# Optimization experiments

Measured on AMD Instinct MI355X. Metric: run time of the kernel, lower is better.

## Reference

```python
import jax, jax.numpy as jnp
import numpy as np

H = 8          # num_heads
NUM_SEEDS = 4  # num_seeds (T = T0 + NUM_SEEDS in training/non_trivial)
NEG_INF = float('-inf')


def setup_inputs() -> dict:
    key = jax.random.key(0)
    ks = jax.random.split(key, 9)
    B, T, L, C = 4, 16, 64, 512
    T0 = T - NUM_SEEDS
    x = jax.random.normal(ks[0], (B, T0 * L, C), dtype=jnp.float32)
    x_ctx = jax.random.normal(ks[1], (B, T, L, C), dtype=jnp.float32)
    dx_ctx = jax.random.normal(ks[2], (B, T, L, C), dtype=jnp.float32)
    ctx_mask = jax.random.randint(ks[3], (B, T), 0, 2).astype(jnp.bool_)
    s = 1.0 / np.sqrt(C)
    qkv_w = jax.random.normal(ks[4], (3 * C, C), dtype=jnp.float32) * s
    k_w = jax.random.normal(ks[5], (C, C), dtype=jnp.float32) * s
    v_w = jax.random.normal(ks[6], (C, C), dtype=jnp.float32) * s
    proj_w = jax.random.normal(ks[7], (C, C), dtype=jnp.float32) * s
    proj_b = jax.random.normal(ks[8], (C,), dtype=jnp.float32) * 0.01
    return {"x": x, "x_ctx": x_ctx, "dx_ctx": dx_ctx, "ctx_mask": ctx_mask,
            "qkv_w": qkv_w, "k_w": k_w, "v_w": v_w, "proj_w": proj_w,
            "proj_b": proj_b}


def reference(x, x_ctx, dx_ctx, ctx_mask, qkv_w, k_w, v_w, proj_w, proj_b):
    B, T, L, C = x_ctx.shape
    T0 = x.shape[1] // L
    hd = C // H
    scale = hd ** (-0.5)

    # qkv for the current (self) tokens: [3, B, H, T0*L, hd]
    qkv = (x @ qkv_w.T).reshape(B, T0 * L, 3, H, hd).transpose(2, 0, 3, 1, 4)
    q, k, v = qkv[0], qkv[1], qkv[2]

    # context keys/values: [B, H, T*L, hd]
    k_ctx = (dx_ctx.reshape(B, T * L, C) @ k_w.T).reshape(B, T * L, H, hd).transpose(0, 2, 1, 3)
    v_ctx = (x_ctx.reshape(B, T * L, C) @ v_w.T).reshape(B, T * L, H, hd).transpose(0, 2, 1, 3)

    # cross-context scores: [B, H, T0*L, T, L]
    attn = (jnp.einsum('bhqd,bhkd->bhqk', q, k_ctx) * scale).reshape(B, H, T0 * L, T, L)

    # context mask: drop whole context frames where ctx_mask is False
    attn = jnp.where(ctx_mask[:, None, None, :, None], attn, NEG_INF)

    # non-trivial temporal mask (training): query frame i can't attend to
    # context frame i + num_seeds
    nt = (jnp.arange(T0)[:, None] + NUM_SEEDS) == jnp.arange(T)[None, :]  # [T0, T]
    attn6 = attn.reshape(B, H, T0, L, T, L)
    attn6 = jnp.where(nt[None, None, :, None, :, None], NEG_INF, attn6)
    attn = attn6.reshape(B, H, T0 * L, T, L)

    # per-frame self attention scores: [B, H, T0, L, L] -> [B, H, T0*L, 1, L]
    q6 = q.reshape(B, H, T0, L, hd)
    k6 = k.reshape(B, H, T0, L, hd)
    self_attn = (jnp.einsum('bhtqd,bhtkd->bhtqk', q6, k6) * scale).reshape(B, H, T0 * L, 1, L)

    # joint softmax over (T+1)*L keys
    attn = jnp.concatenate([attn, self_attn], axis=-2).reshape(B, H, T0 * L, (T + 1) * L)
    attn = jax.nn.softmax(attn, axis=-1)

    # split back: cross part @ v_ctx, self part @ v (per frame)
    out = jnp.einsum('bhqk,bhkd->bhqd', attn[:, :, :, :-L], v_ctx)
    a_self = attn[:, :, :, -L:].reshape(B, H, T0, L, L)
    v6 = v.reshape(B, H, T0, L, hd)
    out = out + jnp.einsum('bhtqk,bhtkd->bhtqd', a_self, v6).reshape(B, H, T0 * L, hd)

    out = out.transpose(0, 2, 1, 3).reshape(B, T0 * L, C)
    return out @ proj_w.T + proj_b
```

## Files before the change

kernel.cpp:

```cpp
#include <hip/hip_runtime.h>
#include <hip/hip_bf16.h>

typedef __attribute__((ext_vector_type(8))) short bf16x8;
typedef __attribute__((ext_vector_type(4))) float f32x4;

#define BB 4
#define TT 16
#define NT0 12
#define LL 64
#define CC 512
#define HH 8
#define HD 64
#define NQ (NT0*LL)
#define NCTX (TT*LL)

#define GPTR(x) ((__attribute__((address_space(1))) void*)(x))
#define SPTR(x) ((__attribute__((address_space(3))) void*)(x))

__device__ __forceinline__ float bf2f(ushort u) {
  union { unsigned int i; float f; } x; x.i = ((unsigned int)u) << 16; return x.f;
}
__device__ __forceinline__ ushort f2bf(float f) {
  union { float f; unsigned int i; } x; x.f = f;
  unsigned int r = x.i + 0x7fffu + ((x.i >> 16) & 1u);
  return (ushort)(r >> 16);
}

__global__ __launch_bounds__(256) void cvt_all(const float* __restrict__ w0,
                                               const float* __restrict__ w1,
                                               const float* __restrict__ w2,
                                               const float* __restrict__ w3,
                                               const float* __restrict__ x,
                                               const float* __restrict__ xc,
                                               const float* __restrict__ dxc,
                                               ushort* __restrict__ dst) {
  long i = (long)blockIdx.x * 256 + threadIdx.x;
  const float* src; long off;
  if (i < 196608)       { src = w0;  off = 0; }
  else if (i < 262144)  { src = w1;  off = 196608; }
  else if (i < 327680)  { src = w2;  off = 262144; }
  else if (i < 393216)  { src = w3;  off = 327680; }
  else if (i < 786432)  { src = x;   off = 393216; }
  else if (i < 1310720) { src = xc;  off = 786432; }
  else                  { src = dxc; off = 1310720; }
  f32x4 v = *(const f32x4*)(src + (i - off) * 4);
  ushort4 o = { f2bf(v[0]), f2bf(v[1]), f2bf(v[2]), f2bf(v[3]) };
  *(ushort4*)(dst + i * 4) = o;
}

__device__ __forceinline__ void gemm128_mac(const ushort* __restrict__ A,
                                            const ushort* __restrict__ W,
                                            int mt, int nt, ushort* lds,
                                            f32x4* acc) {
  int t = threadIdx.x;
  ushort* ldsA = lds;
  ushort* ldsW = lds + 4096;

  int p0 = t, p1 = t + 256;
  int r0 = p0 >> 2, r1 = p1 >> 2;
  int c0 = (p0 & 3) ^ ((r0 >> 1) & 3);
  int c1 = (p1 & 3) ^ ((r1 >> 1) & 3);
  const ushort* ga0 = A + (size_t)(mt * 128 + r0) * 512 + c0 * 8;
  const ushort* ga1 = A + (size_t)(mt * 128 + r1) * 512 + c1 * 8;
  const ushort* gw0 = W + (size_t)(nt * 128 + r0) * 512 + c0 * 8;
  const ushort* gw1 = W + (size_t)(nt * 128 + r1) * 512 + c1 * 8;
  ushort* la0 = ldsA + p0 * 8;
  ushort* la1 = ldsA + p1 * 8;
  ushort* lw0 = ldsW + p0 * 8;
  ushort* lw1 = ldsW + p1 * 8;

  int lane = t & 63, l15 = lane & 15, kg = lane >> 4;
  int wv = t >> 6;
  int mh = (wv >> 1) * 64, nh = (wv & 1) * 64;
  int swz = kg ^ ((l15 >> 1) & 3);
  const ushort* fa = ldsA + (mh + l15) * 32 + swz * 8;
  const ushort* fw = ldsW + (nh + l15) * 32 + swz * 8;

  for (int ks = 0; ks < 16; ++ks) {
    int ko = ks * 32;
    __builtin_amdgcn_global_load_lds(GPTR(ga0 + ko), SPTR(la0), 16, 0, 0);
    __builtin_amdgcn_global_load_lds(GPTR(ga1 + ko), SPTR(la1), 16, 0, 0);
    __builtin_amdgcn_global_load_lds(GPTR(gw0 + ko), SPTR(lw0), 16, 0, 0);
    __builtin_amdgcn_global_load_lds(GPTR(gw1 + ko), SPTR(lw1), 16, 0, 0);
    __syncthreads();
    bf16x8 af[4], wf[4];
#pragma unroll
    for (int i = 0; i < 4; ++i) af[i] = *(const bf16x8*)(fa + i * 512);
#pragma unroll
    for (int i = 0; i < 4; ++i) wf[i] = *(const bf16x8*)(fw + i * 512);
#pragma unroll
    for (int mi = 0; mi < 4; ++mi)
#pragma unroll
      for (int ni = 0; ni < 4; ++ni)
        acc[mi * 4 + ni] =
            __builtin_amdgcn_mfma_f32_16x16x32_bf16(af[mi], wf[ni], acc[mi * 4 + ni], 0, 0, 0);
    __syncthreads();
  }
}

template<int OUTMODE>
__device__ __forceinline__ void gemm128(const ushort* __restrict__ A,
                                        const ushort* __restrict__ W,
                                        ushort* __restrict__ C,
                                        ushort* __restrict__ CT,
                                        float* __restrict__ Cf,
                                        const float* __restrict__ bias,
                                        int mt, int nt, int N, long TM,
                                        ushort* lds) {
  f32x4 acc[16] = {{0,0,0,0},{0,0,0,0},{0,0,0,0},{0,0,0,0},
                   {0,0,0,0},{0,0,0,0},{0,0,0,0},{0,0,0,0},
                   {0,0,0,0},{0,0,0,0},{0,0,0,0},{0,0,0,0},
                   {0,0,0,0},{0,0,0,0},{0,0,0,0},{0,0,0,0}};
  gemm128_mac(A, W, mt, nt, lds, acc);

  int lane = threadIdx.x & 63, l15 = lane & 15, kg = lane >> 4;
  int wv = threadIdx.x >> 6;
  int Rw = mt * 128 + (wv >> 1) * 64;
  int Cw = nt * 128 + (wv & 1) * 64;
#pragma unroll
  for (int mi = 0; mi < 4; ++mi) {
    int row = Rw + mi * 16 + kg * 4;
#pragma unroll
    for (int ni = 0; ni < 4; ++ni) {
      f32x4 v = acc[mi * 4 + ni];
      int col = Cw + ni * 16 + l15;
      if (OUTMODE == 0) {
#pragma unroll
        for (int r = 0; r < 4; ++r) C[(size_t)(row + r) * N + col] = f2bf(v[r]);
      } else if (OUTMODE == 1) {
        ushort4 o = { f2bf(v[0]), f2bf(v[1]), f2bf(v[2]), f2bf(v[3]) };
        *(ushort4*)(CT + (long)col * TM + row) = o;
      } else {
        float bv = bias[col];
#pragma unroll
        for (int r = 0; r < 4; ++r) Cf[(size_t)(row + r) * N + col] = v[r] + bv;
      }
    }
  }
}

__global__ __launch_bounds__(256) void gemm3(const ushort* __restrict__ xb,
                                             const ushort* __restrict__ dxb,
                                             const ushort* __restrict__ xcb,
                                             const ushort* __restrict__ qkvwb,
                                             const ushort* __restrict__ kwb,
                                             const ushort* __restrict__ vwb,
                                             ushort* __restrict__ qkv,
                                             ushort* __restrict__ vselfT,
                                             ushort* __restrict__ kctx,
                                             ushort* __restrict__ vctxT) {
  __shared__ ushort lds[8192];
  int blk = blockIdx.x;
  if (blk < 288) {
    int mt = blk % 24, nt = blk / 24;
    if (nt < 8)
      gemm128<0>(xb, qkvwb, qkv, nullptr, nullptr, nullptr, mt, nt, 1536, 0, lds);
    else
      gemm128<1>(xb, qkvwb, nullptr, vselfT - (size_t)1024 * 3072, nullptr, nullptr,
                 mt, nt, 1536, 3072, lds);
  } else if (blk < 416) {
    int r = blk - 288;
    gemm128<0>(dxb, kwb, kctx, nullptr, nullptr, nullptr, r % 32, r / 32, 512, 0, lds);
  } else {
    int r = blk - 416;
    gemm128<1>(xcb, vwb, nullptr, vctxT, nullptr, nullptr, r % 32, r / 32, 512, 4096, lds);
  }
}

__global__ __launch_bounds__(256) void gemm_proj(const ushort* __restrict__ aout,
                                                 const ushort* __restrict__ pwb,
                                                 const float* __restrict__ bias,
                                                 float* __restrict__ out) {
  __shared__ ushort lds[8192];
  int blk = blockIdx.x;
  gemm128<2>(aout, pwb, nullptr, nullptr, out, bias, blk % 24, blk / 24, 512, 0, lds);
}

__global__ __launch_bounds__(256) void flash_attn(const ushort* __restrict__ qkv,
                                                  const ushort* __restrict__ kctx,
                                                  const ushort* __restrict__ vctxT,
                                                  const ushort* __restrict__ vselfT,
                                                  const int* __restrict__ ctx_mask,
                                                  ushort* __restrict__ aout) {
  __shared__ ushort Pt[4][16 * 72];
  int blk = blockIdx.x;
  int t0 = blk % NT0;
  int h  = (blk / NT0) % HH;
  int b  = blk / (NT0 * HH);
  int tid = threadIdx.x, wv = tid >> 6, lane = tid & 63;
  int l15 = lane & 15, kg = lane >> 4;

  int qrow = b * NQ + t0 * LL + wv * 16 + l15;
  const ushort* qp = qkv + (size_t)qrow * 1536 + h * HD + kg * 8;
  bf16x8 q0 = *(const bf16x8*)qp;
  bf16x8 q1 = *(const bf16x8*)(qp + 32);

  f32x4 acc[4] = {{0,0,0,0},{0,0,0,0},{0,0,0,0},{0,0,0,0}};
  float Mr = -INFINITY, Lr = 0.f;
  ushort* myPt = &Pt[wv][0];

  for (int kt = 0; kt <= TT; ++kt) {
    const ushort* kbase; int kstr;
    if (kt < TT) {
      if (!(ctx_mask[b * TT + kt] != 0 && kt != t0 + 4)) continue;
      kbase = kctx + (size_t)(b * NCTX + kt * LL) * CC + h * HD;
      kstr = CC;
    } else {
      kbase = qkv + (size_t)(b * NQ + t0 * LL) * 1536 + CC + h * HD;
      kstr = 1536;
    }

    f32x4 s[4];
#pragma unroll
    for (int st = 0; st < 4; ++st) {
      const ushort* kp = kbase + (size_t)(st * 16 + l15) * kstr + kg * 8;
      bf16x8 k0 = *(const bf16x8*)kp;
      bf16x8 k1 = *(const bf16x8*)(kp + 32);
      f32x4 z = {0, 0, 0, 0};
      z = __builtin_amdgcn_mfma_f32_16x16x32_bf16(k0, q0, z, 0, 0, 0);
      z = __builtin_amdgcn_mfma_f32_16x16x32_bf16(k1, q1, z, 0, 0, 0);
      s[st] = z * 0.125f;
    }

    float tmax = -INFINITY;
#pragma unroll
    for (int st = 0; st < 4; ++st)
#pragma unroll
      for (int r = 0; r < 4; ++r) tmax = fmaxf(tmax, s[st][r]);
    tmax = fmaxf(tmax, __shfl_xor(tmax, 16, 64));
    tmax = fmaxf(tmax, __shfl_xor(tmax, 32, 64));
    float Mn = fmaxf(Mr, tmax);
    float alpha = __expf(Mr - Mn);
    Mr = Mn;
    float tsum = 0.f;
#pragma unroll
    for (int st = 0; st < 4; ++st)
#pragma unroll
      for (int r = 0; r < 4; ++r) {
        float p = __expf(s[st][r] - Mr);
        s[st][r] = p;
        tsum += p;
      }
    tsum += __shfl_xor(tsum, 16, 64);
    tsum += __shfl_xor(tsum, 32, 64);
    Lr = Lr * alpha + tsum;
#pragma unroll
    for (int d = 0; d < 4; ++d) acc[d] *= alpha;

#pragma unroll
    for (int st = 0; st < 4; ++st) {
      ushort4 pk = { f2bf(s[st][0]), f2bf(s[st][1]), f2bf(s[st][2]), f2bf(s[st][3]) };
      *(ushort4*)(myPt + l15 * 72 + st * 16 + kg * 4) = pk;
    }

    const ushort* vtb; int vtN;
    if (kt < TT) { vtb = vctxT + (size_t)h * HD * (BB * NCTX) + b * NCTX + kt * LL; vtN = BB * NCTX; }
    else         { vtb = vselfT + (size_t)h * HD * (BB * NQ) + b * NQ + t0 * LL;   vtN = BB * NQ; }
#pragma unroll
    for (int kc = 0; kc < 2; ++kc) {
      bf16x8 pb = *(const bf16x8*)(myPt + l15 * 72 + kc * 32 + kg * 8);
#pragma unroll
      for (int d = 0; d < 4; ++d) {
        const ushort* vp = vtb + (size_t)(d * 16 + l15) * vtN + kc * 32 + kg * 8;
        bf16x8 vf = *(const bf16x8*)vp;
        acc[d] = __builtin_amdgcn_mfma_f32_16x16x32_bf16(vf, pb, acc[d], 0, 0, 0);
      }
    }
  }

  float inv = 1.f / Lr;
  int orow = b * NQ + t0 * LL + wv * 16 + l15;
#pragma unroll
  for (int d = 0; d < 4; ++d) {
    ushort4 o = { f2bf(acc[d][0] * inv), f2bf(acc[d][1] * inv),
                  f2bf(acc[d][2] * inv), f2bf(acc[d][3] * inv) };
    *(ushort4*)(aout + (size_t)orow * CC + h * HD + d * 16 + kg * 4) = o;
  }
}

extern "C" void kernel_launch(void* const* d_in, const int* in_sizes, int n_in,
                              void* d_out, int out_size, void* d_ws, size_t ws_size,
                              hipStream_t stream) {
  const float* x        = (const float*)d_in[0];
  const float* x_ctx    = (const float*)d_in[1];
  const float* dx_ctx   = (const float*)d_in[2];
  const int*   ctx_mask = (const int*)d_in[3];
  const float* qkv_w    = (const float*)d_in[4];
  const float* k_w      = (const float*)d_in[5];
  const float* v_w      = (const float*)d_in[6];
  const float* proj_w   = (const float*)d_in[7];
  const float* proj_b   = (const float*)d_in[8];
  float* out = (float*)d_out;

  ushort* ws = (ushort*)d_ws;
  ushort* qkvwb  = ws;
  ushort* kwb    = ws + 786432;
  ushort* vwb    = ws + 1048576;
  ushort* pwb    = ws + 1310720;
  ushort* xb     = ws + 1572864;
  ushort* xcb    = ws + 3145728;
  ushort* dxb    = ws + 5242880;
  ushort* qkv    = ws + 7340032;
  ushort* kctx   = ws + 12058624;
  ushort* vctxT  = ws + 14155776;
  ushort* vselfT = ws + 16252928;
  ushort* aout   = ws + 17825792;

  cvt_all<<<7168, 256, 0, stream>>>(qkv_w, k_w, v_w, proj_w, x, x_ctx, dx_ctx, ws);
  gemm3<<<544, 256, 0, stream>>>(xb, dxb, xcb, qkvwb, kwb, vwb,
                                 qkv, vselfT, kctx, vctxT);
  flash_attn<<<BB * HH * NT0, 256, 0, stream>>>(qkv, kctx, vctxT, vselfT, ctx_mask, aout);
  gemm_proj<<<96, 256, 0, stream>>>(aout, pwb, proj_b, out);
}
```

Baseline: 157.8 us.

## Double GEMM K-step depth and split attention keys across two wave groups

The shared GEMM mainloop now loads 64-wide K slices per step, using 8 steps instead of 16, with a new XOR swizzle and twice the LDS. The goal is to halve the barrier count and give each sync more MFMAs. Flash attention moves to 512 threads, with two wave groups each handling half of the context frames (one also takes the self frame). The two partial softmax states are then merged through LDS. This doubles the waves per attention block, which has only 384 blocks, at the cost of an extra LDS reduction and more LDS per block.

```diff
diff --git a/kernel.cpp b/kernel.cpp
--- a/kernel.cpp
+++ b/kernel.cpp
@@ -54,46 +54,53 @@
                                             f32x4* acc) {
   int t = threadIdx.x;
   ushort* ldsA = lds;
-  ushort* ldsW = lds + 4096;
-
-  int p0 = t, p1 = t + 256;
-  int r0 = p0 >> 2, r1 = p1 >> 2;
-  int c0 = (p0 & 3) ^ ((r0 >> 1) & 3);
-  int c1 = (p1 & 3) ^ ((r1 >> 1) & 3);
-  const ushort* ga0 = A + (size_t)(mt * 128 + r0) * 512 + c0 * 8;
-  const ushort* ga1 = A + (size_t)(mt * 128 + r1) * 512 + c1 * 8;
-  const ushort* gw0 = W + (size_t)(nt * 128 + r0) * 512 + c0 * 8;
-  const ushort* gw1 = W + (size_t)(nt * 128 + r1) * 512 + c1 * 8;
-  ushort* la0 = ldsA + p0 * 8;
-  ushort* la1 = ldsA + p1 * 8;
-  ushort* lw0 = ldsW + p0 * 8;
-  ushort* lw1 = ldsW + p1 * 8;
+  ushort* ldsW = lds + 8192;
+
+  const ushort *gA[4], *gW[4];
+  ushort *lA[4], *lW[4];
+#pragma unroll
+  for (int i = 0; i < 4; ++i) {
+    int p = t + 256 * i;
+    int r = p >> 3, cs = p & 7, c = cs ^ (r & 7);
+    gA[i] = A + (size_t)(mt * 128 + r) * 512 + c * 8;
+    gW[i] = W + (size_t)(nt * 128 + r) * 512 + c * 8;
+    lA[i] = ldsA + p * 8;
+    lW[i] = ldsW + p * 8;
+  }
 
   int lane = t & 63, l15 = lane & 15, kg = lane >> 4;
   int wv = t >> 6;
   int mh = (wv >> 1) * 64, nh = (wv & 1) * 64;
-  int swz = kg ^ ((l15 >> 1) & 3);
-  const ushort* fa = ldsA + (mh + l15) * 32 + swz * 8;
-  const ushort* fw = ldsW + (nh + l15) * 32 + swz * 8;
-
-  for (int ks = 0; ks < 16; ++ks) {
-    int ko = ks * 32;
-    __builtin_amdgcn_global_load_lds(GPTR(ga0 + ko), SPTR(la0), 16, 0, 0);
-    __builtin_amdgcn_global_load_lds(GPTR(ga1 + ko), SPTR(la1), 16, 0, 0);
-    __builtin_amdgcn_global_load_lds(GPTR(gw0 + ko), SPTR(lw0), 16, 0, 0);
-    __builtin_amdgcn_global_load_lds(GPTR(gw1 + ko), SPTR(lw1), 16, 0, 0);
+  int slot0 = kg ^ (l15 & 7);
+  const ushort* fa0 = ldsA + (mh + l15) * 64 + slot0 * 8;
+  const ushort* fa1 = ldsA + (mh + l15) * 64 + (slot0 ^ 4) * 8;
+  const ushort* fw0 = ldsW + (nh + l15) * 64 + slot0 * 8;
+  const ushort* fw1 = ldsW + (nh + l15) * 64 + (slot0 ^ 4) * 8;
+
+  for (int ks = 0; ks < 8; ++ks) {
+    int ko = ks * 64;
+#pragma unroll
+    for (int i = 0; i < 4; ++i) {
+      __builtin_amdgcn_global_load_lds(GPTR(gA[i] + ko), SPTR(lA[i]), 16, 0, 0);
+      __builtin_amdgcn_global_load_lds(GPTR(gW[i] + ko), SPTR(lW[i]), 16, 0, 0);
+    }
     __syncthreads();
-    bf16x8 af[4], wf[4];
-#pragma unroll
-    for (int i = 0; i < 4; ++i) af[i] = *(const bf16x8*)(fa + i * 512);
-#pragma unroll
-    for (int i = 0; i < 4; ++i) wf[i] = *(const bf16x8*)(fw + i * 512);
-#pragma unroll
-    for (int mi = 0; mi < 4; ++mi)
-#pragma unroll
-      for (int ni = 0; ni < 4; ++ni)
-        acc[mi * 4 + ni] =
-            __builtin_amdgcn_mfma_f32_16x16x32_bf16(af[mi], wf[ni], acc[mi * 4 + ni], 0, 0, 0);
+    bf16x8 af[2][4], wf[2][4];
+#pragma unroll
+    for (int i = 0; i < 4; ++i) {
+      af[0][i] = *(const bf16x8*)(fa0 + i * 1024);
+      af[1][i] = *(const bf16x8*)(fa1 + i * 1024);
+      wf[0][i] = *(const bf16x8*)(fw0 + i * 1024);
+      wf[1][i] = *(const bf16x8*)(fw1 + i * 1024);
+    }
+#pragma unroll
+    for (int h = 0; h < 2; ++h)
+#pragma unroll
+      for (int mi = 0; mi < 4; ++mi)
+#pragma unroll
+        for (int ni = 0; ni < 4; ++ni)
+          acc[mi * 4 + ni] = __builtin_amdgcn_mfma_f32_16x16x32_bf16(
+              af[h][mi], wf[h][ni], acc[mi * 4 + ni], 0, 0, 0);
     __syncthreads();
   }
 }
@@ -149,7 +156,7 @@
                                              ushort* __restrict__ vselfT,
                                              ushort* __restrict__ kctx,
                                              ushort* __restrict__ vctxT) {
-  __shared__ ushort lds[8192];
+  __shared__ ushort lds[16384];
   int blk = blockIdx.x;
   if (blk < 288) {
     int mt = blk % 24, nt = blk / 24;
@@ -171,26 +178,27 @@
                                                  const ushort* __restrict__ pwb,
                                                  const float* __restrict__ bias,
                                                  float* __restrict__ out) {
-  __shared__ ushort lds[8192];
+  __shared__ ushort lds[16384];
   int blk = blockIdx.x;
   gemm128<2>(aout, pwb, nullptr, nullptr, out, bias, blk % 24, blk / 24, 512, 0, lds);
 }
 
-__global__ __launch_bounds__(256) void flash_attn(const ushort* __restrict__ qkv,
+__global__ __launch_bounds__(512) void flash_attn(const ushort* __restrict__ qkv,
                                                   const ushort* __restrict__ kctx,
                                                   const ushort* __restrict__ vctxT,
                                                   const ushort* __restrict__ vselfT,
                                                   const int* __restrict__ ctx_mask,
                                                   ushort* __restrict__ aout) {
-  __shared__ ushort Pt[4][16 * 72];
+  __shared__ ushort Pt[8][1152];
   int blk = blockIdx.x;
   int t0 = blk % NT0;
   int h  = (blk / NT0) % HH;
   int b  = blk / (NT0 * HH);
   int tid = threadIdx.x, wv = tid >> 6, lane = tid & 63;
+  int qg = wv & 3, kside = wv >> 2;
   int l15 = lane & 15, kg = lane >> 4;
 
-  int qrow = b * NQ + t0 * LL + wv * 16 + l15;
+  int qrow = b * NQ + t0 * LL + qg * 16 + l15;
   const ushort* qp = qkv + (size_t)qrow * 1536 + h * HD + kg * 8;
   bf16x8 q0 = *(const bf16x8*)qp;
   bf16x8 q1 = *(const bf16x8*)(qp + 32);
@@ -199,9 +207,12 @@
   float Mr = -INFINITY, Lr = 0.f;
   ushort* myPt = &Pt[wv][0];
 
-  for (int kt = 0; kt <= TT; ++kt) {
+  int nkt = kside ? 8 : 9;
+  for (int ki = 0; ki < nkt; ++ki) {
+    bool self = (!kside) && (ki == 8);
+    int kt = kside ? (8 + ki) : ki;
     const ushort* kbase; int kstr;
-    if (kt < TT) {
+    if (!self) {
       if (!(ctx_mask[b * TT + kt] != 0 && kt != t0 + 4)) continue;
       kbase = kctx + (size_t)(b * NCTX + kt * LL) * CC + h * HD;
       kstr = CC;
@@ -254,8 +265,8 @@
     }
 
     const ushort* vtb; int vtN;
-    if (kt < TT) { vtb = vctxT + (size_t)h * HD * (BB * NCTX) + b * NCTX + kt * LL; vtN = BB * NCTX; }
-    else         { vtb = vselfT + (size_t)h * HD * (BB * NQ) + b * NQ + t0 * LL;   vtN = BB * NQ; }
+    if (!self) { vtb = vctxT + (size_t)h * HD * (BB * NCTX) + b * NCTX + kt * LL; vtN = BB * NCTX; }
+    else       { vtb = vselfT + (size_t)h * HD * (BB * NQ) + b * NQ + t0 * LL;   vtN = BB * NQ; }
 #pragma unroll
     for (int kc = 0; kc < 2; ++kc) {
       bf16x8 pb = *(const bf16x8*)(myPt + l15 * 72 + kc * 32 + kg * 8);
@@ -268,13 +279,29 @@
     }
   }
 
-  float inv = 1.f / Lr;
-  int orow = b * NQ + t0 * LL + wv * 16 + l15;
-#pragma unroll
-  for (int d = 0; d < 4; ++d) {
-    ushort4 o = { f2bf(acc[d][0] * inv), f2bf(acc[d][1] * inv),
-                  f2bf(acc[d][2] * inv), f2bf(acc[d][3] * inv) };
-    *(ushort4*)(aout + (size_t)orow * CC + h * HD + d * 16 + kg * 4) = o;
+  __syncthreads();
+  float* base = (float*)&Pt[0][0] + (size_t)qg * 1152;
+  if (kside) {
+#pragma unroll
+    for (int d = 0; d < 4; ++d) *(f32x4*)(base + lane * 16 + d * 4) = acc[d];
+    base[1024 + lane] = Mr;
+    base[1088 + lane] = Lr;
+  }
+  __syncthreads();
+  if (!kside) {
+    float M1 = base[1024 + lane], L1 = base[1088 + lane];
+    float Mn = fmaxf(Mr, M1);
+    float a0 = __expf(Mr - Mn), a1 = __expf(M1 - Mn);
+    float inv = 1.f / (Lr * a0 + L1 * a1);
+    int orow = b * NQ + t0 * LL + qg * 16 + l15;
+#pragma unroll
+    for (int d = 0; d < 4; ++d) {
+      f32x4 o1 = *(const f32x4*)(base + lane * 16 + d * 4);
+      f32x4 v = acc[d] * a0 + o1 * a1;
+      ushort4 o = { f2bf(v[0] * inv), f2bf(v[1] * inv),
+                    f2bf(v[2] * inv), f2bf(v[3] * inv) };
+      *(ushort4*)(aout + (size_t)orow * CC + h * HD + d * 16 + kg * 4) = o;
+    }
   }
 }
 
@@ -309,6 +336,6 @@
   cvt_all<<<7168, 256, 0, stream>>>(qkv_w, k_w, v_w, proj_w, x, x_ctx, dx_ctx, ws);
   gemm3<<<544, 256, 0, stream>>>(xb, dxb, xcb, qkvwb, kwb, vwb,
                                  qkv, vselfT, kctx, vctxT);
-  flash_attn<<<BB * HH * NT0, 256, 0, stream>>>(qkv, kctx, vctxT, vselfT, ctx_mask, aout);
+  flash_attn<<<BB * HH * NT0, 512, 0, stream>>>(qkv, kctx, vctxT, vselfT, ctx_mask, aout);
   gemm_proj<<<96, 256, 0, stream>>>(aout, pwb, proj_b, out);
 }
```

After: 160.9 us. Within noise of the previous version (+2.0%).

## Split flash attention across key frames with split-K softmax merge

Applied to the files above, without the earlier changes.

Each attention block now covers half of a frame's queries. Its 8 waves split the 17 key tiles into 4 groups, and the partial max, sum and accumulator results are merged through shared memory. This raises the block count from 384 to 768 and shortens each wave's serial loop over key frames, improving occupancy and latency hiding on the many CUs. In exchange it adds a shared-memory reduction, two barriers, and uneven work per group (the first group also handles the self tile).

```diff
diff --git a/kernel.cpp b/kernel.cpp
--- a/kernel.cpp
+++ b/kernel.cpp
@@ -176,32 +176,38 @@
   gemm128<2>(aout, pwb, nullptr, nullptr, out, bias, blk % 24, blk / 24, 512, 0, lds);
 }
 
-__global__ __launch_bounds__(256) void flash_attn(const ushort* __restrict__ qkv,
+__global__ __launch_bounds__(512) void flash_attn(const ushort* __restrict__ qkv,
                                                   const ushort* __restrict__ kctx,
                                                   const ushort* __restrict__ vctxT,
                                                   const ushort* __restrict__ vselfT,
                                                   const int* __restrict__ ctx_mask,
                                                   ushort* __restrict__ aout) {
-  __shared__ ushort Pt[4][16 * 72];
+  __shared__ float smem[6912];
   int blk = blockIdx.x;
-  int t0 = blk % NT0;
-  int h  = (blk / NT0) % HH;
-  int b  = blk / (NT0 * HH);
+  int qh = blk & 1;
+  int rest = blk >> 1;
+  int t0 = rest % NT0;
+  int h  = (rest / NT0) % HH;
+  int b  = rest / (NT0 * HH);
   int tid = threadIdx.x, wv = tid >> 6, lane = tid & 63;
+  int qg = wv & 1, ks = wv >> 1;
   int l15 = lane & 15, kg = lane >> 4;
 
-  int qrow = b * NQ + t0 * LL + wv * 16 + l15;
+  int qrow = b * NQ + t0 * LL + qh * 32 + qg * 16 + l15;
   const ushort* qp = qkv + (size_t)qrow * 1536 + h * HD + kg * 8;
   bf16x8 q0 = *(const bf16x8*)qp;
   bf16x8 q1 = *(const bf16x8*)(qp + 32);
 
   f32x4 acc[4] = {{0,0,0,0},{0,0,0,0},{0,0,0,0},{0,0,0,0}};
   float Mr = -INFINITY, Lr = 0.f;
-  ushort* myPt = &Pt[wv][0];
-
-  for (int kt = 0; kt <= TT; ++kt) {
+  ushort* myPt = (ushort*)smem + wv * 1152;
+
+  int nkt = (ks == 0) ? 5 : 4;
+  for (int ki = 0; ki < nkt; ++ki) {
+    bool self = (ks == 0) && (ki == 4);
+    int kt = ks * 4 + ki;
     const ushort* kbase; int kstr;
-    if (kt < TT) {
+    if (!self) {
       if (!(ctx_mask[b * TT + kt] != 0 && kt != t0 + 4)) continue;
       kbase = kctx + (size_t)(b * NCTX + kt * LL) * CC + h * HD;
       kstr = CC;
@@ -254,8 +260,8 @@
     }
 
     const ushort* vtb; int vtN;
-    if (kt < TT) { vtb = vctxT + (size_t)h * HD * (BB * NCTX) + b * NCTX + kt * LL; vtN = BB * NCTX; }
-    else         { vtb = vselfT + (size_t)h * HD * (BB * NQ) + b * NQ + t0 * LL;   vtN = BB * NQ; }
+    if (!self) { vtb = vctxT + (size_t)h * HD * (BB * NCTX) + b * NCTX + kt * LL; vtN = BB * NCTX; }
+    else       { vtb = vselfT + (size_t)h * HD * (BB * NQ) + b * NQ + t0 * LL;   vtN = BB * NQ; }
 #pragma unroll
     for (int kc = 0; kc < 2; ++kc) {
       bf16x8 pb = *(const bf16x8*)(myPt + l15 * 72 + kc * 32 + kg * 8);
@@ -268,13 +274,47 @@
     }
   }
 
-  float inv = 1.f / Lr;
-  int orow = b * NQ + t0 * LL + wv * 16 + l15;
-#pragma unroll
-  for (int d = 0; d < 4; ++d) {
-    ushort4 o = { f2bf(acc[d][0] * inv), f2bf(acc[d][1] * inv),
-                  f2bf(acc[d][2] * inv), f2bf(acc[d][3] * inv) };
-    *(ushort4*)(aout + (size_t)orow * CC + h * HD + d * 16 + kg * 4) = o;
+  __syncthreads();
+  if (ks) {
+    float* reg = smem + (size_t)(qg * 3 + ks - 1) * 1152;
+#pragma unroll
+    for (int d = 0; d < 4; ++d) *(f32x4*)(reg + lane * 16 + d * 4) = acc[d];
+    reg[1024 + lane] = Mr;
+    reg[1088 + lane] = Lr;
+  }
+  __syncthreads();
+  if (!ks) {
+    float Mj[3], Lj[3];
+    float Ms = Mr;
+#pragma unroll
+    for (int j = 0; j < 3; ++j) {
+      const float* reg = smem + (size_t)(qg * 3 + j) * 1152;
+      Mj[j] = reg[1024 + lane];
+      Lj[j] = reg[1088 + lane];
+      Ms = fmaxf(Ms, Mj[j]);
+    }
+    float a0 = __expf(Mr - Ms);
+    float Ls = Lr * a0;
+    f32x4 o[4];
+#pragma unroll
+    for (int d = 0; d < 4; ++d) o[d] = acc[d] * a0;
+#pragma unroll
+    for (int j = 0; j < 3; ++j) {
+      const float* reg = smem + (size_t)(qg * 3 + j) * 1152;
+      float aj = __expf(Mj[j] - Ms);
+      Ls += Lj[j] * aj;
+#pragma unroll
+      for (int d = 0; d < 4; ++d)
+        o[d] += *(const f32x4*)(reg + lane * 16 + d * 4) * aj;
+    }
+    float inv = 1.f / Ls;
+    int orow = b * NQ + t0 * LL + qh * 32 + qg * 16 + l15;
+#pragma unroll
+    for (int d = 0; d < 4; ++d) {
+      ushort4 ov = { f2bf(o[d][0] * inv), f2bf(o[d][1] * inv),
+                     f2bf(o[d][2] * inv), f2bf(o[d][3] * inv) };
+      *(ushort4*)(aout + (size_t)orow * CC + h * HD + d * 16 + kg * 4) = ov;
+    }
   }
 }
 
@@ -309,6 +349,6 @@
   cvt_all<<<7168, 256, 0, stream>>>(qkv_w, k_w, v_w, proj_w, x, x_ctx, dx_ctx, ws);
   gemm3<<<544, 256, 0, stream>>>(xb, dxb, xcb, qkvwb, kwb, vwb,
                                  qkv, vselfT, kctx, vctxT);
-  flash_attn<<<BB * HH * NT0, 256, 0, stream>>>(qkv, kctx, vctxT, vselfT, ctx_mask, aout);
+  flash_attn<<<768, 512, 0, stream>>>(qkv, kctx, vctxT, vselfT, ctx_mask, aout);
   gemm_proj<<<96, 256, 0, stream>>>(aout, pwb, proj_b, out);
 }
```

New measurement: 151.4 us. -4.1%, faster.
